# Optimization experiments

Hardware: AMD Instinct MI355X
Metric: run time of the kernel (lower is better)

The kernel has to match this reference:

```python
import jax, jax.numpy as jnp
import numpy as np


def setup_inputs() -> dict:
    key = jax.random.key(0)
    k1, k2 = jax.random.split(key)
    b, c, h, w = 32, 3, 32, 32
    N = 100000
    x = jax.random.normal(k1, (b, c, h, w), dtype=jnp.float32)
    train_data = jax.random.normal(k2, (N, c, h, w), dtype=jnp.float32)
    # linear beta schedule (diffusion default): betas in [1e-4, 0.02], T=1000
    betas = jnp.linspace(1e-4, 0.02, 1000, dtype=jnp.float32)
    alphas_cumprod = jnp.cumprod(1.0 - betas)
    t = 150  # t_start < t < t_end branch -> epsilon_star_batch
    return {"x": x, "train_data": train_data, "alphas_cumprod": alphas_cumprod, "t": t}


def reference(x, train_data, alphas_cumprod, t):
    # epsilon_star_batch: softmax-weighted average of train set under
    # Gaussian kernel exp(-||x - sqrt(ab)*x0||^2 / (2*(1-ab)))
    ab = alphas_cumprod[t]
    s = jnp.sqrt(ab)
    one_minus = 1.0 - ab
    b = x.shape[0]
    N = train_data.shape[0]
    xf = x.reshape(b, -1)            # [b, D]
    tf = train_data.reshape(N, -1)   # [N, D]
    # ||x - s*x0||^2 = ||x||^2 - 2 s x.x0 + s^2 ||x0||^2 (avoids [b,N,D] blowup)
    x_sq = jnp.sum(xf * xf, axis=1, keepdims=True)      # [b,1]
    t_sq = jnp.sum(tf * tf, axis=1)                     # [N]
    cross = xf @ tf.T                                   # [b,N]
    logits = -(x_sq - 2.0 * s * cross + ab * t_sq) / (2.0 * one_minus)  # [b,N]
    wts = jax.nn.softmax(logits, axis=1)                # [b,N]
    weighted_x = (wts @ tf).reshape(x.shape)            # [b,c,h,w]
    inv = 1.0 / jnp.sqrt(one_minus)
    return x * inv - s * inv * weighted_x
```

## Files before the change

kernel.cpp:

```cpp
#include <hip/hip_runtime.h>

#define BATCH  32
#define DIM    3072
#define NTRAIN 100000
#define NBLK1  3125

#define KCH    128
#define NCH    24
#define ROWB   512
#define BUFB   (32 * ROWB)

#define NSEG   8
#define SEGJ   12500
#define SEGCAP 1024
#define THRESH 25.0f
#define MPROW  3136

typedef __bf16 bf16x8 __attribute__((ext_vector_type(8)));
typedef float  f32x16 __attribute__((ext_vector_type(16)));
typedef unsigned short u16;
typedef unsigned int   u32;

union F8 { u16 us[8]; u32 ui[4]; uint4 u4; bf16x8 bf; };

__device__ __forceinline__ u16   bft(float f){ return (u16)(__float_as_uint(f) >> 16); }
__device__ __forceinline__ float bfh(float f){ return __uint_as_float(__float_as_uint(f) & 0xFFFF0000u); }

__global__ __launch_bounds__(256) void k0_split_x_v2(
        const float* __restrict__ x, u16* __restrict__ xfh, u16* __restrict__ xfl) {
    int task = blockIdx.x * 256 + threadIdx.x;
    if (task >= 12288) return;
    int kb  = task >> 6;
    int rem = task & 63;
    int r   = rem >> 1;
    int g   = rem & 1;
    const float* src = x + r * DIM + kb * 16 + g * 8;
    float4 A = *(const float4*)(src);
    float4 B = *(const float4*)(src + 4);
    float fv[8] = {A.x, A.y, A.z, A.w, B.x, B.y, B.z, B.w};
    F8 h, l;
#pragma unroll
    for (int e = 0; e < 8; ++e) {
        h.us[e] = bft(fv[e]);
        l.us[e] = bft(fv[e] - bfh(fv[e]));
    }
    size_t off = (size_t)kb * 512 + r * 16 + g * 8;
    *(uint4*)(xfh + off) = h.u4;
    *(uint4*)(xfl + off) = l.u4;
}

__global__ __launch_bounds__(256) void k1_logits_v7(
        const float* __restrict__ train,
        const u16* __restrict__ xfh, const u16* __restrict__ xfl,
        const float* __restrict__ alphas, const int* __restrict__ tptr,
        float* __restrict__ logits, float* __restrict__ m_part) {
    __shared__ __align__(16) char smem[3 * BUFB];
    const int tid  = threadIdx.x;
    const int lane = tid & 63;
    const int w    = tid >> 6;
    const int l31  = lane & 31;
    const int g    = lane >> 5;
    const int jt0  = blockIdx.x * 32;

    const float ab = alphas[tptr[0]];
    const float s  = sqrtf(ab);
    const float om = 1.0f - ab;
    const float c1 = s / om;
    const float c2 = ab / (2.0f * om);

    const char* gblk = (const char*)train + (size_t)jt0 * (DIM * 4);

    f32x16 acc;
#pragma unroll
    for (int r = 0; r < 16; ++r) acc[r] = 0.0f;
    float tsqp = 0.0f;

    auto stage = [&](int buf, int c) {
#pragma unroll
        for (int i = 0; i < 4; ++i) {
            const int R0 = w * 8 + i * 2;
            const int r  = R0 + (lane >> 5);
            const u32 colS = (u32)((lane & 31) << 4) ^ ((u32)(r & 7) << 4);
            const char* src = gblk + (size_t)r * (DIM * 4) + c * (KCH * 4) + colS;
            char* dst = smem + buf * BUFB + R0 * ROWB;
            __builtin_amdgcn_global_load_lds(
                (const __attribute__((address_space(1))) unsigned int*)src,
                (__attribute__((address_space(3))) unsigned int*)dst,
                16, 0, 0);
        }
    };
    auto ldx = [&](int c, F8* ah, F8* al) {
#pragma unroll
        for (int s4 = 0; s4 < 2; ++s4) {
            const int kb16 = c * 8 + w * 2 + s4;
            const size_t off = (size_t)kb16 * 512 + l31 * 16 + g * 8;
            ah[s4].u4 = *(const uint4*)(xfh + off);
            al[s4].u4 = *(const uint4*)(xfl + off);
        }
    };

    F8 ahc[2], alc[2];
    stage(0, 0);
    __builtin_amdgcn_sched_barrier(0);
    ldx(0, ahc, alc);
    __builtin_amdgcn_sched_barrier(0);
    stage(1, 1);

    const u32 rsw = ((u32)(l31 & 7)) << 4;

    for (int c = 0; c < NCH; ++c) {
        if (c < NCH - 1) {
            asm volatile("s_waitcnt vmcnt(4)\n\ts_barrier" ::: "memory");
        } else {
            asm volatile("s_waitcnt vmcnt(0)\n\ts_barrier" ::: "memory");
        }

        F8 ahn[2], aln[2];
        if (c + 1 < NCH) ldx(c + 1, ahn, aln);
        __builtin_amdgcn_sched_barrier(0);
        if (c + 2 < NCH) stage((c + 2) % 3, c + 2);
        __builtin_amdgcn_sched_barrier(0);

        const char* lb = smem + (c % 3) * BUFB + l31 * ROWB;
#pragma unroll
        for (int s4 = 0; s4 < 2; ++s4) {
            const u32 kb0 = (u32)(w * 128 + s4 * 64 + g * 32);
            const float4 f0 = *(const float4*)(lb + ((kb0      ) ^ rsw));
            const float4 f1 = *(const float4*)(lb + ((kb0 + 16u) ^ rsw));
            float fv[8] = {f0.x, f0.y, f0.z, f0.w, f1.x, f1.y, f1.z, f1.w};
            F8 bh, bl;
#pragma unroll
            for (int e = 0; e < 8; ++e) {
                float f = fv[e];
                bh.us[e] = bft(f);
                bl.us[e] = bft(f - bfh(f));
                tsqp = fmaf(f, f, tsqp);
            }
            acc = __builtin_amdgcn_mfma_f32_32x32x16_bf16(ahc[s4].bf, bh.bf, acc, 0, 0, 0);
            acc = __builtin_amdgcn_mfma_f32_32x32x16_bf16(alc[s4].bf, bh.bf, acc, 0, 0, 0);
            acc = __builtin_amdgcn_mfma_f32_32x32x16_bf16(ahc[s4].bf, bl.bf, acc, 0, 0, 0);
        }
        if (c + 1 < NCH) {
            ahc[0] = ahn[0]; ahc[1] = ahn[1];
            alc[0] = aln[0]; alc[1] = aln[1];
        }
    }
    __syncthreads();

    tsqp += __shfl_xor(tsqp, 32);
    float* red = (float*)smem;
    if (w > 0) {
        float* dp = red + ((w - 1) * 64 + lane) * 16;
#pragma unroll
        for (int r = 0; r < 16; ++r) dp[r] = acc[r];
    }
    if (g == 0) red[3072 + w * 32 + l31] = tsqp;
    __syncthreads();
    if (w == 0) {
#pragma unroll
        for (int q = 0; q < 3; ++q) {
            const float* sp = red + (q * 64 + lane) * 16;
#pragma unroll
            for (int r = 0; r < 16; ++r) acc[r] += sp[r];
        }
        const float tsq = red[3072 + l31] + red[3072 + 32 + l31]
                        + red[3072 + 64 + l31] + red[3072 + 96 + l31];
        float lg[16];
#pragma unroll
        for (int r = 0; r < 16; ++r) {
            lg[r] = c1 * acc[r] - c2 * tsq;
            int brow = (r & 3) + 8 * (r >> 2) + 4 * g;
            logits[(size_t)brow * NTRAIN + jt0 + l31] = lg[r];
        }
#pragma unroll
        for (int d = 1; d < 32; d <<= 1)
#pragma unroll
            for (int r = 0; r < 16; ++r)
                lg[r] = fmaxf(lg[r], __shfl_xor(lg[r], d));
        if (l31 == 0) {
#pragma unroll
            for (int r = 0; r < 16; ++r) {
                int brow = (r & 3) + 8 * (r >> 2) + 4 * g;
                m_part[(size_t)brow * MPROW + blockIdx.x] = lg[r];
            }
        }
    }
}

__global__ __launch_bounds__(256) void k2a_rowmax_v2(
        const float* __restrict__ m_part, float* __restrict__ m) {
    const int b = blockIdx.x;
    float mx = -3.0e38f;
    for (int i = threadIdx.x; i < NBLK1; i += 256)
        mx = fmaxf(mx, m_part[(size_t)b * MPROW + i]);
    __shared__ float red[256];
    red[threadIdx.x] = mx;
    __syncthreads();
    for (int off = 128; off > 0; off >>= 1) {
        if (threadIdx.x < (unsigned)off)
            red[threadIdx.x] = fmaxf(red[threadIdx.x], red[threadIdx.x + off]);
        __syncthreads();
    }
    if (threadIdx.x == 0) m[b] = red[0];
}

__global__ __launch_bounds__(256) void k2b_select(
        const float* __restrict__ logits, const float* __restrict__ m,
        int* __restrict__ idx, float* __restrict__ wts,
        int* __restrict__ cnt, float* __restrict__ lsum) {
    const int b   = blockIdx.x >> 3;
    const int seg = blockIdx.x & 7;
    const int tid = threadIdx.x;
    const float mb = m[b];
    const int j0 = seg * SEGJ;
    const int j1 = min(j0 + SEGJ, NTRAIN);
    const float* lrow = logits + (size_t)b * NTRAIN;

    int mycnt = 0;
    for (int j = j0 + tid; j < j1; j += 256)
        if (lrow[j] >= mb - THRESH) ++mycnt;

    __shared__ int   soff[257];
    __shared__ float ssum[256];
    soff[tid + 1] = mycnt;
    __syncthreads();
    if (tid == 0) {
        soff[0] = 0;
        for (int t = 1; t <= 256; ++t) soff[t] += soff[t - 1];
    }
    __syncthreads();

    int off = soff[tid];
    const int base = (b * NSEG + seg) * SEGCAP;
    float mysum = 0.0f;
    for (int j = j0 + tid; j < j1; j += 256) {
        float lg = lrow[j];
        if (lg >= mb - THRESH) {
            float wv = __expf(lg - mb);
            mysum += wv;
            if (off < SEGCAP) { idx[base + off] = j; wts[base + off] = wv; }
            ++off;
        }
    }
    ssum[tid] = mysum;
    __syncthreads();
    if (tid == 0) {
        float Ls = 0.0f;
        for (int t = 0; t < 256; ++t) Ls += ssum[t];
        lsum[b * NSEG + seg] = Ls;
        cnt[b * NSEG + seg]  = min(soff[256], SEGCAP);
    }
}

__global__ __launch_bounds__(256) void k3_gather(
        const float* __restrict__ x, const float* __restrict__ train,
        const int* __restrict__ idx, const float* __restrict__ wts,
        const int* __restrict__ cnt, const float* __restrict__ lsum,
        const float* __restrict__ alphas, const int* __restrict__ tptr,
        float* __restrict__ out) {
    const int blk  = blockIdx.x;
    const int b    = blk / 12;
    const int dseg = blk % 12;
    const int d    = dseg * 256 + threadIdx.x;

    const float ab  = alphas[tptr[0]];
    const float s   = sqrtf(ab);
    const float om  = 1.0f - ab;
    const float inv = 1.0f / sqrtf(om);

    float L = 0.0f;
#pragma unroll
    for (int sg = 0; sg < NSEG; ++sg) L += lsum[b * NSEG + sg];

    float acc = 0.0f;
    for (int sg = 0; sg < NSEG; ++sg) {
        const int n    = cnt[b * NSEG + sg];
        const int base = (b * NSEG + sg) * SEGCAP;
        for (int i = 0; i < n; ++i) {
            const int   j = idx[base + i];
            const float w = wts[base + i];
            acc = fmaf(w, train[(size_t)j * DIM + d], acc);
        }
    }
    const size_t o = (size_t)b * DIM + d;
    out[o] = inv * x[o] - s * inv * (acc / L);
}

extern "C" void kernel_launch(void* const* d_in, const int* in_sizes, int n_in,
                              void* d_out, int out_size, void* d_ws, size_t ws_size,
                              hipStream_t stream) {
    const float* x      = (const float*)d_in[0];
    const float* train  = (const float*)d_in[1];
    const float* alphas = (const float*)d_in[2];
    const int*   tptr   = (const int*)d_in[3];
    float* out = (float*)d_out;

    char* ws = (char*)d_ws;
    float* logits = (float*)ws;
    float* m_part = (float*)(ws + 12800000);
    float* m_arr  = (float*)(ws + 13201408);
    float* lsum   = (float*)(ws + 13201536);
    int*   cnt    = (int*)(ws + 13202560);
    int*   idx    = (int*)(ws + 13203584);
    float* wts    = (float*)(ws + 14252160);
    u16*   xfh    = (u16*)(ws + 15300736);
    u16*   xfl    = (u16*)(ws + 15497344);

    k0_split_x_v2<<<48, 256, 0, stream>>>(x, xfh, xfl);
    k1_logits_v7<<<NBLK1, 256, 0, stream>>>(train, xfh, xfl, alphas, tptr,
                                            logits, m_part);
    k2a_rowmax_v2<<<BATCH, 256, 0, stream>>>(m_part, m_arr);
    k2b_select<<<BATCH * NSEG, 256, 0, stream>>>(logits, m_arr, idx, wts, cnt, lsum);
    k3_gather<<<BATCH * 12, 256, 0, stream>>>(x, train, idx, wts, cnt, lsum,
                                              alphas, tptr, out);
}
```

Measured before the change: 305.9 us.

## Split-K the tail tiles of logits kernel and fold rowmax into select

Measured after the change: 293.7 us. -4.0%, faster.

```diff
diff --git a/kernel.cpp b/kernel.cpp
--- a/kernel.cpp
+++ b/kernel.cpp
@@ -3,10 +3,13 @@
 #define BATCH  32
 #define DIM    3072
 #define NTRAIN 100000
-#define NBLK1  3125
+#define NTILE1 3125
+#define NFULL  3072
+#define NREM   53
 
 #define KCH    128
 #define NCH    24
+#define NCHQ   6
 #define ROWB   512
 #define BUFB   (32 * ROWB)
 
@@ -49,18 +52,30 @@
     *(uint4*)(xfl + off) = l.u4;
 }
 
-__global__ __launch_bounds__(256) void k1_logits_v7(
+__global__ __launch_bounds__(256) void k1_logits_v8(
         const float* __restrict__ train,
         const u16* __restrict__ xfh, const u16* __restrict__ xfl,
         const float* __restrict__ alphas, const int* __restrict__ tptr,
-        float* __restrict__ logits, float* __restrict__ m_part) {
+        float* __restrict__ logits, float* __restrict__ m_part,
+        float* __restrict__ qpart) {
     __shared__ __align__(16) char smem[3 * BUFB];
     const int tid  = threadIdx.x;
     const int lane = tid & 63;
     const int w    = tid >> 6;
     const int l31  = lane & 31;
     const int g    = lane >> 5;
-    const int jt0  = blockIdx.x * 32;
+    const int bid  = blockIdx.x;
+
+    int tile, cbase, nch, qp = 0;
+    if (bid < NFULL) { tile = bid; cbase = 0; nch = NCH; }
+    else {
+        int rem = bid - NFULL;
+        tile  = NFULL + (rem >> 2);
+        qp    = rem & 3;
+        cbase = qp * NCHQ;
+        nch   = NCHQ;
+    }
+    const int jt0 = tile * 32;
 
     const float ab = alphas[tptr[0]];
     const float s  = sqrtf(ab);
@@ -100,28 +115,28 @@
     };
 
     F8 ahc[2], alc[2];
-    stage(0, 0);
+    stage(0, cbase);
     __builtin_amdgcn_sched_barrier(0);
-    ldx(0, ahc, alc);
+    ldx(cbase, ahc, alc);
     __builtin_amdgcn_sched_barrier(0);
-    stage(1, 1);
+    stage(1, cbase + 1);
 
     const u32 rsw = ((u32)(l31 & 7)) << 4;
 
-    for (int c = 0; c < NCH; ++c) {
-        if (c < NCH - 1) {
+    for (int i = 0; i < nch; ++i) {
+        if (i < nch - 1) {
             asm volatile("s_waitcnt vmcnt(4)\n\ts_barrier" ::: "memory");
         } else {
             asm volatile("s_waitcnt vmcnt(0)\n\ts_barrier" ::: "memory");
         }
 
         F8 ahn[2], aln[2];
-        if (c + 1 < NCH) ldx(c + 1, ahn, aln);
+        if (i + 1 < nch) ldx(cbase + i + 1, ahn, aln);
         __builtin_amdgcn_sched_barrier(0);
-        if (c + 2 < NCH) stage((c + 2) % 3, c + 2);
+        if (i + 2 < nch) stage((i + 2) % 3, cbase + i + 2);
         __builtin_amdgcn_sched_barrier(0);
 
-        const char* lb = smem + (c % 3) * BUFB + l31 * ROWB;
+        const char* lb = smem + (i % 3) * BUFB + l31 * ROWB;
 #pragma unroll
         for (int s4 = 0; s4 < 2; ++s4) {
             const u32 kb0 = (u32)(w * 128 + s4 * 64 + g * 32);
@@ -140,7 +155,7 @@
             acc = __builtin_amdgcn_mfma_f32_32x32x16_bf16(alc[s4].bf, bh.bf, acc, 0, 0, 0);
             acc = __builtin_amdgcn_mfma_f32_32x32x16_bf16(ahc[s4].bf, bl.bf, acc, 0, 0, 0);
         }
-        if (c + 1 < NCH) {
+        if (i + 1 < nch) {
             ahc[0] = ahn[0]; ahc[1] = ahn[1];
             alc[0] = aln[0]; alc[1] = aln[1];
         }
@@ -165,53 +180,87 @@
         }
         const float tsq = red[3072 + l31] + red[3072 + 32 + l31]
                         + red[3072 + 64 + l31] + red[3072 + 96 + l31];
-        float lg[16];
-#pragma unroll
-        for (int r = 0; r < 16; ++r) {
-            lg[r] = c1 * acc[r] - c2 * tsq;
-            int brow = (r & 3) + 8 * (r >> 2) + 4 * g;
-            logits[(size_t)brow * NTRAIN + jt0 + l31] = lg[r];
-        }
-#pragma unroll
-        for (int d = 1; d < 32; d <<= 1)
-#pragma unroll
-            for (int r = 0; r < 16; ++r)
-                lg[r] = fmaxf(lg[r], __shfl_xor(lg[r], d));
-        if (l31 == 0) {
+        if (bid < NFULL) {
+            float lg[16];
+#pragma unroll
+            for (int r = 0; r < 16; ++r) {
+                lg[r] = c1 * acc[r] - c2 * tsq;
+                int brow = (r & 3) + 8 * (r >> 2) + 4 * g;
+                logits[(size_t)brow * NTRAIN + jt0 + l31] = lg[r];
+            }
+#pragma unroll
+            for (int d = 1; d < 32; d <<= 1)
+#pragma unroll
+                for (int r = 0; r < 16; ++r)
+                    lg[r] = fmaxf(lg[r], __shfl_xor(lg[r], d));
+            if (l31 == 0) {
+#pragma unroll
+                for (int r = 0; r < 16; ++r) {
+                    int brow = (r & 3) + 8 * (r >> 2) + 4 * g;
+                    m_part[(size_t)brow * MPROW + bid] = lg[r];
+                }
+            }
+        } else {
+            const int t = tile - NFULL;
 #pragma unroll
             for (int r = 0; r < 16; ++r) {
                 int brow = (r & 3) + 8 * (r >> 2) + 4 * g;
-                m_part[(size_t)brow * MPROW + blockIdx.x] = lg[r];
+                qpart[(((size_t)t * 4 + qp) * 32 + brow) * 32 + l31]
+                    = c1 * acc[r] - c2 * tsq;
             }
         }
     }
 }
 
-__global__ __launch_bounds__(256) void k2a_rowmax_v2(
-        const float* __restrict__ m_part, float* __restrict__ m) {
-    const int b = blockIdx.x;
+__global__ __launch_bounds__(256) void k1c_combine(
+        const float* __restrict__ qpart, float* __restrict__ logits,
+        float* __restrict__ m_part) {
+    const int t    = blockIdx.x;
+    const int brow = threadIdx.x >> 3;
+    const int jg   = threadIdx.x & 7;
+    float v[4];
     float mx = -3.0e38f;
-    for (int i = threadIdx.x; i < NBLK1; i += 256)
-        mx = fmaxf(mx, m_part[(size_t)b * MPROW + i]);
-    __shared__ float red[256];
-    red[threadIdx.x] = mx;
-    __syncthreads();
-    for (int off = 128; off > 0; off >>= 1) {
-        if (threadIdx.x < (unsigned)off)
-            red[threadIdx.x] = fmaxf(red[threadIdx.x], red[threadIdx.x + off]);
-        __syncthreads();
-    }
-    if (threadIdx.x == 0) m[b] = red[0];
+#pragma unroll
+    for (int jj = 0; jj < 4; ++jj) {
+        const int j31 = jg * 4 + jj;
+        float sum = 0.0f;
+#pragma unroll
+        for (int p = 0; p < 4; ++p)
+            sum += qpart[(((size_t)t * 4 + p) * 32 + brow) * 32 + j31];
+        v[jj] = sum;
+        mx = fmaxf(mx, sum);
+    }
+    *(float4*)(logits + (size_t)brow * NTRAIN + NFULL * 32 + t * 32 + jg * 4)
+        = make_float4(v[0], v[1], v[2], v[3]);
+    mx = fmaxf(mx, __shfl_xor(mx, 1));
+    mx = fmaxf(mx, __shfl_xor(mx, 2));
+    mx = fmaxf(mx, __shfl_xor(mx, 4));
+    if (jg == 0) m_part[(size_t)brow * MPROW + NFULL + t] = mx;
 }
 
 __global__ __launch_bounds__(256) void k2b_select(
-        const float* __restrict__ logits, const float* __restrict__ m,
+        const float* __restrict__ logits, const float* __restrict__ m_part,
         int* __restrict__ idx, float* __restrict__ wts,
         int* __restrict__ cnt, float* __restrict__ lsum) {
     const int b   = blockIdx.x >> 3;
     const int seg = blockIdx.x & 7;
     const int tid = threadIdx.x;
-    const float mb = m[b];
+
+    __shared__ int   soff[257];
+    __shared__ float ssum[256];
+
+    float mx = -3.0e38f;
+    for (int i = tid; i < NTILE1; i += 256)
+        mx = fmaxf(mx, m_part[(size_t)b * MPROW + i]);
+    ssum[tid] = mx;
+    __syncthreads();
+    for (int off = 128; off > 0; off >>= 1) {
+        if (tid < off) ssum[tid] = fmaxf(ssum[tid], ssum[tid + off]);
+        __syncthreads();
+    }
+    const float mb = ssum[0];
+    __syncthreads();
+
     const int j0 = seg * SEGJ;
     const int j1 = min(j0 + SEGJ, NTRAIN);
     const float* lrow = logits + (size_t)b * NTRAIN;
@@ -220,8 +269,6 @@
     for (int j = j0 + tid; j < j1; j += 256)
         if (lrow[j] >= mb - THRESH) ++mycnt;
 
-    __shared__ int   soff[257];
-    __shared__ float ssum[256];
     soff[tid + 1] = mycnt;
     __syncthreads();
     if (tid == 0) {
@@ -244,10 +291,12 @@
     }
     ssum[tid] = mysum;
     __syncthreads();
+    for (int o2 = 128; o2 > 0; o2 >>= 1) {
+        if (tid < o2) ssum[tid] += ssum[tid + o2];
+        __syncthreads();
+    }
     if (tid == 0) {
-        float Ls = 0.0f;
-        for (int t = 0; t < 256; ++t) Ls += ssum[t];
-        lsum[b * NSEG + seg] = Ls;
+        lsum[b * NSEG + seg] = ssum[0];
         cnt[b * NSEG + seg]  = min(soff[256], SEGCAP);
     }
 }
@@ -298,19 +347,19 @@
     char* ws = (char*)d_ws;
     float* logits = (float*)ws;
     float* m_part = (float*)(ws + 12800000);
-    float* m_arr  = (float*)(ws + 13201408);
-    float* lsum   = (float*)(ws + 13201536);
-    int*   cnt    = (int*)(ws + 13202560);
-    int*   idx    = (int*)(ws + 13203584);
-    float* wts    = (float*)(ws + 14252160);
-    u16*   xfh    = (u16*)(ws + 15300736);
-    u16*   xfl    = (u16*)(ws + 15497344);
+    float* qpart  = (float*)(ws + 13201408);
+    float* lsum   = (float*)(ws + 14069760);
+    int*   cnt    = (int*)(ws + 14070784);
+    int*   idx    = (int*)(ws + 14071808);
+    float* wts    = (float*)(ws + 15120384);
+    u16*   xfh    = (u16*)(ws + 16168960);
+    u16*   xfl    = (u16*)(ws + 16365568);
 
     k0_split_x_v2<<<48, 256, 0, stream>>>(x, xfh, xfl);
-    k1_logits_v7<<<NBLK1, 256, 0, stream>>>(train, xfh, xfl, alphas, tptr,
-                                            logits, m_part);
-    k2a_rowmax_v2<<<BATCH, 256, 0, stream>>>(m_part, m_arr);
-    k2b_select<<<BATCH * NSEG, 256, 0, stream>>>(logits, m_arr, idx, wts, cnt, lsum);
+    k1_logits_v8<<<NFULL + NREM * 4, 256, 0, stream>>>(train, xfh, xfl, alphas,
+                                                       tptr, logits, m_part, qpart);
+    k1c_combine<<<NREM, 256, 0, stream>>>(qpart, logits, m_part);
+    k2b_select<<<BATCH * NSEG, 256, 0, stream>>>(logits, m_part, idx, wts, cnt, lsum);
     k3_gather<<<BATCH * 12, 256, 0, stream>>>(x, train, idx, wts, cnt, lsum,
                                               alphas, tptr, out);
 }
```
